# Optimization experiments

Hardware: AMD Instinct MI355X
Metric: run time of the kernel (lower is better)

Reference implementation:

```python
import jax, jax.numpy as jnp
import numpy as np

B, N, D = 128, 512, 128   # batch, nodes (= patch_len / time_window_size), feature dim (d_model_patch)
EPS = 1e-5                # torch BatchNorm1d default eps
SLOPE = 0.01              # torch F.leaky_relu default negative_slope
DIAG_INF = 1e8            # eyes_like * 100000000.0 in Dot_Graph_Construction_weights


def mask_matrix(T, decay):
    # Faithful replication of Mask_Matrix: slices i*T:(i+1)*T on a [T,T] array
    # are empty for i >= 1, so the result is all ones; we replicate exactly.
    A = np.ones((T, T), np.float32)
    for i in range(T):
        v = 0
        for r in range(i, T):
            A[i * T:(i + 1) * T, r * T:(r + 1) * T] *= decay ** v
            v += 1
        v = 0
        for r in range(i + 1):
            A[i * T:(i + 1) * T, (i - r) * T:(i - r + 1) * T] *= decay ** v
            v += 1
    return A


def setup_inputs() -> dict:
    key = jax.random.key(0)
    ks = jax.random.split(key, 3)
    s = 1.0 / np.sqrt(D)  # torch Linear default init scale
    return {
        "x": jax.random.normal(ks[0], (B, N, D), jnp.float32),
        "W_map": jax.random.uniform(ks[1], (D, D), jnp.float32, -s, s),
        "b_map": jnp.zeros((D,), jnp.float32),
        "W_theta": jax.random.uniform(ks[2], (D, D), jnp.float32, -s, s),
        "b_theta": jnp.zeros((D,), jnp.float32),
        "gamma_in": jnp.ones((D,), jnp.float32),
        "beta_in": jnp.zeros((D,), jnp.float32),
        "gamma_out": jnp.ones((D,), jnp.float32),
        "beta_out": jnp.zeros((D,), jnp.float32),
        "pre_relation": jnp.asarray(mask_matrix(N, 0.9)),
    }


def leaky_relu(x):
    return jnp.where(x >= 0, x, SLOPE * x)


def batchnorm(x, gamma, beta):
    # x: [B, N, C]; BatchNorm1d over channel C (training-mode batch stats,
    # matching torch transpose -> BN -> transpose pattern).
    mean = x.mean((0, 1))
    var = x.var((0, 1))
    return (x - mean) * jax.lax.rsqrt(var + EPS) * gamma + beta


def reference(x, W_map, b_map, W_theta, b_theta, gamma_in, beta_in,
              gamma_out, beta_out, pre_relation):
    # --- Dot_Graph_Construction_weights ---
    nf = x @ W_map + b_map                         # [B,N,D]
    adj = jnp.einsum('bnd,bmd->bnm', nf, nf)       # [B,N,N]
    eye = jnp.eye(N, dtype=x.dtype)
    adj = leaky_relu(adj - eye * DIAG_INF)
    adj = jax.nn.softmax(adj, axis=-1) + eye
    # --- decay mask (all-ones, computed faithfully) ---
    adj = adj * pre_relation
    # --- input BN ---
    xb = batchnorm(x, gamma_in, beta_in)
    # --- MPNN_mk_v2, k=1 ---
    h = jnp.einsum('bnm,bmd->bnd', adj, xb) @ W_theta + b_theta
    h = batchnorm(h, gamma_out, beta_out)
    return leaky_relu(h)                           # [B,N,D]
```

## Files before the change

### kernel.cpp

```cpp
#include <hip/hip_runtime.h>
#include <hip/hip_bf16.h>

#define B_ 128
#define N_ 512
#define D_ 128
#define M_ (B_ * N_)
#define LDSP 136

typedef unsigned short u16;
typedef short s8v __attribute__((ext_vector_type(8)));
typedef __bf16 bf8v __attribute__((ext_vector_type(8)));
typedef float f4v __attribute__((ext_vector_type(4)));

__device__ __forceinline__ float b2f(u16 v) {
  return __uint_as_float(((unsigned)v) << 16);
}
__device__ __forceinline__ u16 f2b(float f) {
  unsigned u = __float_as_uint(f);
  return (u16)((u + 0x7fffu + ((u >> 16) & 1u)) >> 16);
}
__device__ __forceinline__ void split2(float v, u16& hi, u16& lo) {
  hi = f2b(v);
  lo = f2b(v - b2f(hi));
}
__device__ __forceinline__ u16* swzK(u16* base, int row, int col) {
  return (u16*)((char*)base + row * 256 + ((col * 2) ^ ((row & 15) << 4)));
}
__device__ __forceinline__ u16* swz64(u16* base, int row, int col) {
  return (u16*)((char*)base + row * 128 + ((col * 2) ^ ((row & 7) << 4)));
}
__device__ __forceinline__ int kperm(int c) {
  return (c & 3) + ((c >> 2) & 1) * 16 + ((c >> 3) & 3) * 4 + (c >> 5) * 32;
}
__device__ __forceinline__ void derive_ss(const float* __restrict__ stats,
                                          const float* __restrict__ gamma,
                                          const float* __restrict__ beta,
                                          float* sSS, int t) {
  if (t < 128) {
    float mean = stats[t] * (1.0f / (float)M_);
    float var  = stats[128 + t] * (1.0f / (float)M_) - mean * mean;
    float sc = gamma[t] * rsqrtf(var + 1e-5f);
    sSS[t] = sc;
    sSS[128 + t] = beta[t] - mean * sc;
  }
}

__global__ __launch_bounds__(256) void prologue(const float* __restrict__ Wa,
                                                const float* __restrict__ Wb,
                                                u16* __restrict__ WTah, u16* __restrict__ WTal,
                                                u16* __restrict__ WTbh,
                                                const float* __restrict__ X,
                                                float* __restrict__ stats) {
  const int t = threadIdx.x;
  const int id = blockIdx.x;
  if (id < 128) {
    const int idx = (id & 63) * 256 + t;
    const int k = idx >> 7, j = idx & 127;
    if (id < 64) {
      u16 hh, ll;
      split2(Wa[idx], hh, ll);
      WTah[j * 128 + k] = hh;
      WTal[j * 128 + k] = ll;
    } else {
      WTbh[j * 128 + k] = f2b(Wb[idx]);
    }
    return;
  }
  const int g = t & 31;
  const int h = t >> 5;
  const size_t r0 = (size_t)(id - 128) * 256;
  float s[4] = {0.f, 0.f, 0.f, 0.f}, q[4] = {0.f, 0.f, 0.f, 0.f};
  for (int r = h; r < 256; r += 8) {
    float4 v = *(const float4*)&X[(r0 + r) * D_ + g * 4];
    s[0] += v.x; q[0] += v.x * v.x;
    s[1] += v.y; q[1] += v.y * v.y;
    s[2] += v.z; q[2] += v.z * v.z;
    s[3] += v.w; q[3] += v.w * v.w;
  }
  __shared__ float red[256][8];
#pragma unroll
  for (int j = 0; j < 4; ++j) { red[t][j] = s[j]; red[t][4 + j] = q[j]; }
  __syncthreads();
  if (t < 32) {
    float S[4] = {0.f, 0.f, 0.f, 0.f}, Q[4] = {0.f, 0.f, 0.f, 0.f};
    for (int hh = 0; hh < 8; ++hh) {
      const float* p = red[hh * 32 + t];
#pragma unroll
      for (int j = 0; j < 4; ++j) { S[j] += p[j]; Q[j] += p[4 + j]; }
    }
#pragma unroll
    for (int j = 0; j < 4; ++j) {
      atomicAdd(&stats[t * 4 + j], S[j]);
      atomicAdd(&stats[128 + t * 4 + j], Q[j]);
    }
  }
}

__global__ __launch_bounds__(256) void xbT_kernel(const float* __restrict__ X,
                                                  const float* __restrict__ stats,
                                                  const float* __restrict__ gamma,
                                                  const float* __restrict__ beta,
                                                  u16* __restrict__ XBT) {
  __shared__ __align__(16) u16 sT[128][LDSP];
  __shared__ float sSS[256];
  const int t = threadIdx.x;
  const int b = blockIdx.x >> 2;
  const int n0 = (blockIdx.x & 3) * 128;
  const size_t xbase = (size_t)b * N_ * D_;
  const size_t tbase = (size_t)b * D_ * N_;
  derive_ss(stats, gamma, beta, sSS, t);
  __syncthreads();
  {
    const int r = t >> 1, c0 = (t & 1) * 64;
#pragma unroll
    for (int i = 0; i < 16; ++i) {
      const int c = c0 + i * 4;
      float4 v = *(const float4*)&X[xbase + (size_t)(n0 + r) * D_ + c];
      sT[c + 0][r] = f2b(v.x * sSS[c + 0] + sSS[128 + c + 0]);
      sT[c + 1][r] = f2b(v.y * sSS[c + 1] + sSS[128 + c + 1]);
      sT[c + 2][r] = f2b(v.z * sSS[c + 2] + sSS[128 + c + 2]);
      sT[c + 3][r] = f2b(v.w * sSS[c + 3] + sSS[128 + c + 3]);
    }
  }
  __syncthreads();
  {
    const int d = t >> 1, nc = (t & 1) * 64;
#pragma unroll
    for (int i = 0; i < 8; ++i) {
      u16 o[8];
#pragma unroll
      for (int e = 0; e < 8; ++e) {
        const int L = nc + i * 8 + e;
        o[e] = sT[d][kperm(L & 63) + (L & 64)];
      }
      *(s8v*)&XBT[tbase + (size_t)d * N_ + n0 + nc + i * 8] = *(const s8v*)o;
    }
  }
}

__global__ __launch_bounds__(256, 2) void gemm1(const float* __restrict__ A,
                                                const u16* __restrict__ WTh,
                                                const u16* __restrict__ WTl,
                                                const float* __restrict__ bias,
                                                u16* __restrict__ Ch, u16* __restrict__ Cl) {
  __shared__ __align__(16) u16 sWh[128][LDSP];
  __shared__ __align__(16) u16 sWl[128][LDSP];
  const int t = threadIdx.x;
  const int wv = t >> 6, ln = t & 63, l16 = ln & 15, kg = ln >> 4;
  const size_t row0 = (size_t)blockIdx.x * 128;

#pragma unroll
  for (int i = 0; i < 8; ++i) {
    int o = t * 8 + i * 2048;
    int rr = o >> 7, cc = o & 127;
    *(s8v*)&sWh[rr][cc] = *(const s8v*)&WTh[o];
    *(s8v*)&sWl[rr][cc] = *(const s8v*)&WTl[o];
  }

  bf8v ah[2][4], al[2][4];
#pragma unroll
  for (int rf = 0; rf < 2; ++rf) {
    const size_t row = row0 + wv * 32 + rf * 16 + l16;
#pragma unroll
    for (int kt = 0; kt < 4; ++kt) {
      const float* p = &A[row * D_ + kt * 32 + kg * 8];
      float4 v0 = *(const float4*)p;
      float4 v1 = *(const float4*)(p + 4);
      u16 hh[8], ll[8];
      split2(v0.x, hh[0], ll[0]); split2(v0.y, hh[1], ll[1]);
      split2(v0.z, hh[2], ll[2]); split2(v0.w, hh[3], ll[3]);
      split2(v1.x, hh[4], ll[4]); split2(v1.y, hh[5], ll[5]);
      split2(v1.z, hh[6], ll[6]); split2(v1.w, hh[7], ll[7]);
      ah[rf][kt] = *(const bf8v*)hh;
      al[rf][kt] = *(const bf8v*)ll;
    }
  }
  __syncthreads();

  f4v acc[2][8];
#pragma unroll
  for (int rf = 0; rf < 2; ++rf)
#pragma unroll
    for (int jf = 0; jf < 8; ++jf) acc[rf][jf] = f4v{0.f, 0.f, 0.f, 0.f};

#pragma unroll
  for (int kt = 0; kt < 4; ++kt) {
    const int k0 = kt * 32 + kg * 8;
#pragma unroll
    for (int jf = 0; jf < 8; ++jf) {
      bf8v bh = *(const bf8v*)&sWh[jf * 16 + l16][k0];
      bf8v bl = *(const bf8v*)&sWl[jf * 16 + l16][k0];
      acc[0][jf] = __builtin_amdgcn_mfma_f32_16x16x32_bf16(ah[0][kt], bh, acc[0][jf], 0, 0, 0);
      acc[0][jf] = __builtin_amdgcn_mfma_f32_16x16x32_bf16(al[0][kt], bh, acc[0][jf], 0, 0, 0);
      acc[0][jf] = __builtin_amdgcn_mfma_f32_16x16x32_bf16(ah[0][kt], bl, acc[0][jf], 0, 0, 0);
      acc[1][jf] = __builtin_amdgcn_mfma_f32_16x16x32_bf16(ah[1][kt], bh, acc[1][jf], 0, 0, 0);
      acc[1][jf] = __builtin_amdgcn_mfma_f32_16x16x32_bf16(al[1][kt], bh, acc[1][jf], 0, 0, 0);
      acc[1][jf] = __builtin_amdgcn_mfma_f32_16x16x32_bf16(ah[1][kt], bl, acc[1][jf], 0, 0, 0);
    }
  }

#pragma unroll
  for (int rf = 0; rf < 2; ++rf) {
#pragma unroll
    for (int reg = 0; reg < 4; ++reg) {
      const int row = wv * 32 + rf * 16 + kg * 4 + reg;
#pragma unroll
      for (int jf = 0; jf < 8; ++jf) {
        const int col = jf * 16 + l16;
        float v = acc[rf][jf][reg] + bias[col];
        u16 hh, ll;
        split2(v, hh, ll);
        Ch[(row0 + row) * D_ + col] = hh;
        Cl[(row0 + row) * D_ + col] = ll;
      }
    }
  }
}

__global__ __launch_bounds__(256, 2) void gemm2(const u16* __restrict__ A,
                                                const u16* __restrict__ WTh,
                                                const float* __restrict__ bias,
                                                u16* __restrict__ C,
                                                float* __restrict__ stats) {
  __shared__ __align__(16) u16 sWh[128][LDSP];
  __shared__ float sSum[128], sSq[128];
  const int t = threadIdx.x;
  const int wv = t >> 6, ln = t & 63, l16 = ln & 15, kg = ln >> 4;
  const size_t row0 = (size_t)blockIdx.x * 128;

  if (t < 128) { sSum[t] = 0.f; sSq[t] = 0.f; }
#pragma unroll
  for (int i = 0; i < 8; ++i) {
    int o = t * 8 + i * 2048;
    *(s8v*)&sWh[o >> 7][o & 127] = *(const s8v*)&WTh[o];
  }

  bf8v a[2][4];
#pragma unroll
  for (int rf = 0; rf < 2; ++rf) {
    const size_t row = row0 + wv * 32 + rf * 16 + l16;
#pragma unroll
    for (int kt = 0; kt < 4; ++kt)
      a[rf][kt] = *(const bf8v*)&A[row * D_ + kt * 32 + kg * 8];
  }
  __syncthreads();

  f4v acc[2][8];
#pragma unroll
  for (int rf = 0; rf < 2; ++rf)
#pragma unroll
    for (int jf = 0; jf < 8; ++jf) acc[rf][jf] = f4v{0.f, 0.f, 0.f, 0.f};

#pragma unroll
  for (int kt = 0; kt < 4; ++kt) {
    const int k0 = kt * 32 + kg * 8;
#pragma unroll
    for (int jf = 0; jf < 8; ++jf) {
      bf8v bh = *(const bf8v*)&sWh[jf * 16 + l16][k0];
      acc[0][jf] = __builtin_amdgcn_mfma_f32_16x16x32_bf16(a[0][kt], bh, acc[0][jf], 0, 0, 0);
      acc[1][jf] = __builtin_amdgcn_mfma_f32_16x16x32_bf16(a[1][kt], bh, acc[1][jf], 0, 0, 0);
    }
  }

  float cs[8], cq[8];
#pragma unroll
  for (int jf = 0; jf < 8; ++jf) { cs[jf] = 0.f; cq[jf] = 0.f; }
#pragma unroll
  for (int rf = 0; rf < 2; ++rf) {
#pragma unroll
    for (int reg = 0; reg < 4; ++reg) {
      const int row = wv * 32 + rf * 16 + kg * 4 + reg;
#pragma unroll
      for (int jf = 0; jf < 8; ++jf) {
        const int col = jf * 16 + l16;
        u16 hb = f2b(acc[rf][jf][reg] + bias[col]);
        C[(row0 + row) * D_ + col] = hb;
        float vr = b2f(hb);
        cs[jf] += vr;
        cq[jf] += vr * vr;
      }
    }
  }
#pragma unroll
  for (int jf = 0; jf < 8; ++jf) {
    cs[jf] += __shfl_xor(cs[jf], 16); cq[jf] += __shfl_xor(cq[jf], 16);
    cs[jf] += __shfl_xor(cs[jf], 32); cq[jf] += __shfl_xor(cq[jf], 32);
  }
  if (kg == 0) {
#pragma unroll
    for (int jf = 0; jf < 8; ++jf) {
      atomicAdd(&sSum[jf * 16 + l16], cs[jf]);
      atomicAdd(&sSq[jf * 16 + l16], cq[jf]);
    }
  }
  __syncthreads();
  if (t < 128) {
    atomicAdd(&stats[t], sSum[t]);
    atomicAdd(&stats[128 + t], sSq[t]);
  }
}

__global__ __launch_bounds__(512, 4) void attn_kernel(const u16* __restrict__ NFH,
                                                      const u16* __restrict__ NFL,
                                                      const u16* __restrict__ XBT,
                                                      const float* __restrict__ X,
                                                      const float* __restrict__ stats,
                                                      const float* __restrict__ gamma,
                                                      const float* __restrict__ beta,
                                                      u16* __restrict__ ATT) {
  __shared__ __align__(16) u16 pool[17408];
  __shared__ float sSS[256];
  u16* sKh = pool;
  u16* sVT = pool + 8192;
  const int t = threadIdx.x;
  const int wv = t >> 6, ln = t & 63, l16 = ln & 15, kg = ln >> 4;
  const int id = blockIdx.x;
  const int b = (id & 7) + (id >> 5) * 8;
  const int r0 = ((id >> 3) & 3) * 128;
  const size_t base  = (size_t)b * N_ * D_;
  const size_t baseT = (size_t)b * D_ * N_;

  derive_ss(stats, gamma, beta, sSS, t);

  bf8v qh[4], ql[4];
  {
    const size_t qoff = base + (size_t)(r0 + wv * 16 + l16) * D_ + kg * 8;
#pragma unroll
    for (int kt = 0; kt < 4; ++kt) {
      qh[kt] = *(const bf8v*)&NFH[qoff + kt * 32];
      ql[kt] = *(const bf8v*)&NFL[qoff + kt * 32];
    }
  }

  const int kr = t >> 3, kc = (t & 7) * 16;
  const int vd = t >> 2, vc = (t & 3) * 16;
  const u16* gKh = &NFH[base + (size_t)kr * D_ + kc];
  const u16* gV  = &XBT[baseT + (size_t)vd * N_ + vc];
  s8v rh0 = *(const s8v*)gKh, rh1 = *(const s8v*)(gKh + 8);
  s8v rv0 = *(const s8v*)gV,  rv1 = *(const s8v*)(gV + 8);

  float m = -3e38f, l = 0.f;
  f4v accO[8];
#pragma unroll
  for (int df = 0; df < 8; ++df) accO[df] = f4v{0.f, 0.f, 0.f, 0.f};

  for (int j0 = 0; j0 < N_; j0 += 64) {
    *(s8v*)swzK(sKh, kr, kc)      = rh0;
    *(s8v*)swzK(sKh, kr, kc + 8)  = rh1;
    *(s8v*)swz64(sVT, vd, vc)     = rv0;
    *(s8v*)swz64(sVT, vd, vc + 8) = rv1;
    __syncthreads();
    if (j0 + 64 < N_) {
      const int jn = j0 + 64;
      rh0 = *(const s8v*)(gKh + (size_t)jn * D_);
      rh1 = *(const s8v*)(gKh + (size_t)jn * D_ + 8);
      rv0 = *(const s8v*)(gV + jn);
      rv1 = *(const s8v*)(gV + jn + 8);
    }

    f4v accS[4];
#pragma unroll
    for (int jf = 0; jf < 4; ++jf) accS[jf] = f4v{0.f, 0.f, 0.f, 0.f};
    __builtin_amdgcn_s_setprio(1);
#pragma unroll
    for (int kt = 0; kt < 4; ++kt) {
      const int k0 = kt * 32 + kg * 8;
#pragma unroll
      for (int jf = 0; jf < 4; ++jf) {
        bf8v kh_ = *(const bf8v*)swzK(sKh, jf * 16 + l16, k0);
        accS[jf] = __builtin_amdgcn_mfma_f32_16x16x32_bf16(kh_, qh[kt], accS[jf], 0, 0, 0);
        accS[jf] = __builtin_amdgcn_mfma_f32_16x16x32_bf16(kh_, ql[kt], accS[jf], 0, 0, 0);
      }
    }
    __builtin_amdgcn_s_setprio(0);

    const int qg = r0 + wv * 16 + l16;
    float mx = -3e38f;
#pragma unroll
    for (int jf = 0; jf < 4; ++jf) {
#pragma unroll
      for (int reg = 0; reg < 4; ++reg) {
        const int kk = j0 + jf * 16 + kg * 4 + reg;
        float sv = accS[jf][reg];
        if (kk == qg) sv -= 1e8f;
        sv = (sv >= 0.f) ? sv : 0.01f * sv;
        accS[jf][reg] = sv;
        mx = fmaxf(mx, sv);
      }
    }
    mx = fmaxf(mx, __shfl_xor(mx, 16));
    mx = fmaxf(mx, __shfl_xor(mx, 32));
    const bool resc = !__all(mx - m <= 8.0f);
    const float mnew = resc ? fmaxf(m, mx) : m;
    float rs = 0.f;
#pragma unroll
    for (int jf = 0; jf < 4; ++jf) {
#pragma unroll
      for (int reg = 0; reg < 4; ++reg) {
        const float p = __expf(accS[jf][reg] - mnew);
        accS[jf][reg] = p;
        rs += p;
      }
    }
    rs += __shfl_xor(rs, 16);
    rs += __shfl_xor(rs, 32);
    if (resc) {
      const float scl = __expf(m - mnew);
      l = l * scl + rs;
      m = mnew;
#pragma unroll
      for (int df = 0; df < 8; ++df) accO[df] = accO[df] * scl;
    } else {
      l += rs;
    }

    u16 pk0[8], pk1[8];
#pragma unroll
    for (int e = 0; e < 8; ++e) {
      pk0[e] = f2b(accS[(e >> 2)][e & 3]);
      pk1[e] = f2b(accS[2 + (e >> 2)][e & 3]);
    }
    bf8v pb0 = *(const bf8v*)pk0;
    bf8v pb1 = *(const bf8v*)pk1;

    __builtin_amdgcn_s_setprio(1);
#pragma unroll
    for (int kt2 = 0; kt2 < 2; ++kt2) {
      const int k0 = kt2 * 32 + kg * 8;
      const bf8v pb = kt2 ? pb1 : pb0;
#pragma unroll
      for (int df = 0; df < 8; ++df) {
        bf8v av = *(const bf8v*)swz64(sVT, df * 16 + l16, k0);
        accO[df] = __builtin_amdgcn_mfma_f32_16x16x32_bf16(av, pb, accO[df], 0, 0, 0);
      }
    }
    __builtin_amdgcn_s_setprio(0);
    __syncthreads();
  }

  const float inv = 1.0f / l;
  u16* sOut = pool;
#pragma unroll
  for (int df = 0; df < 8; ++df) {
#pragma unroll
    for (int reg = 0; reg < 4; ++reg) {
      const int d = df * 16 + kg * 4 + reg;
      sOut[d * 136 + wv * 16 + l16] = f2b(accO[df][reg] * inv);
    }
  }
  __syncthreads();
  {
    const int q = t >> 2, c0 = (t & 3) * 32;
    const size_t orow = base + (size_t)(r0 + q) * D_;
#pragma unroll
    for (int i = 0; i < 4; ++i) {
      u16 o[8];
#pragma unroll
      for (int e = 0; e < 8; ++e) {
        const int d = c0 + i * 8 + e;
        const float ov = b2f(sOut[d * 136 + q]);
        const float xb = X[orow + d] * sSS[d] + sSS[128 + d];
        o[e] = f2b(ov + xb);
      }
      *(s8v*)&ATT[orow + c0 + i * 8] = *(const s8v*)o;
    }
  }
}

__global__ __launch_bounds__(256) void affine_out(const u16* __restrict__ H,
                                                  const float* __restrict__ stats,
                                                  const float* __restrict__ gamma,
                                                  const float* __restrict__ beta,
                                                  float* __restrict__ Y) {
  __shared__ float sSS[256];
  const int t = threadIdx.x;
  derive_ss(stats, gamma, beta, sSS, t);
  __syncthreads();
  const size_t idx = (size_t)blockIdx.x * 256 + t;
  const int c0 = (int)(idx & 15) * 8;
  s8v v = *(const s8v*)&H[idx * 8];
  float o[8];
#pragma unroll
  for (int e = 0; e < 8; ++e) {
    float x = b2f((u16)v[e]);
    float y = x * sSS[c0 + e] + sSS[128 + c0 + e];
    o[e] = (y >= 0.f) ? y : 0.01f * y;
  }
  *(float4*)&Y[idx * 8]     = make_float4(o[0], o[1], o[2], o[3]);
  *(float4*)&Y[idx * 8 + 4] = make_float4(o[4], o[5], o[6], o[7]);
}

extern "C" void kernel_launch(void* const* d_in, const int* in_sizes, int n_in,
                              void* d_out, int out_size, void* d_ws, size_t ws_size,
                              hipStream_t stream) {
  const float* x         = (const float*)d_in[0];
  const float* W_map     = (const float*)d_in[1];
  const float* b_map     = (const float*)d_in[2];
  const float* W_theta   = (const float*)d_in[3];
  const float* b_theta   = (const float*)d_in[4];
  const float* gamma_in  = (const float*)d_in[5];
  const float* beta_in   = (const float*)d_in[6];
  const float* gamma_out = (const float*)d_in[7];
  const float* beta_out  = (const float*)d_in[8];
  float* out = (float*)d_out;

  char* ws = (char*)d_ws;
  float* stats_x = (float*)ws;
  float* stats_h = (float*)(ws + 1024);
  u16* WT1h = (u16*)(ws + 2048);
  u16* WT1l = WT1h + 128 * 128;
  u16* WT2h = WT1l + 128 * 128;
  const size_t BUF = (size_t)M_ * D_;
  u16* nfh = WT2h + 128 * 128;
  u16* nfl = nfh + BUF;

  u16* xbT  = (u16*)d_out;
  u16* attO = (u16*)d_out + BUF;

  hipMemsetAsync(ws, 0, 2048, stream);

  prologue<<<384, 256, 0, stream>>>(W_map, W_theta, WT1h, WT1l, WT2h, x, stats_x);
  gemm1<<<512, 256, 0, stream>>>(x, WT1h, WT1l, b_map, nfh, nfl);
  xbT_kernel<<<512, 256, 0, stream>>>(x, stats_x, gamma_in, beta_in, xbT);
  attn_kernel<<<512, 512, 0, stream>>>(nfh, nfl, xbT, x, stats_x, gamma_in, beta_in, attO);
  gemm2<<<512, 256, 0, stream>>>(attO, WT2h, b_theta, nfh, stats_h);
  affine_out<<<4096, 256, 0, stream>>>(nfh, stats_h, gamma_out, beta_out, out);
}
```

Baseline: 158.1 us.

## Fuse xbT into gemm1, stage GEMM outputs via LDS, simplify attention inner loop

Removes the separate xbT kernel: gemm1 now computes the normalized transposed bf16 input from its already-loaded hi/lo A fragments and writes XBT, avoiding a second read of x. gemm1 and gemm2 stage outputs in LDS and write coalesced 16-byte rows instead of scattered 2-byte stores. In attention, the diagonal-mask comparison runs only for the tile containing the query row, and the P conversion uses packed v_cvt_pk_bf16_f32. Reconstructing x from hi+lo bf16 may differ slightly from the fp32 original, and the extra syncs and LDS reuse add some overhead to gemm1.

```diff
diff --git a/kernel.cpp b/kernel.cpp
--- a/kernel.cpp
+++ b/kernel.cpp
@@ -11,6 +11,7 @@
 typedef short s8v __attribute__((ext_vector_type(8)));
 typedef __bf16 bf8v __attribute__((ext_vector_type(8)));
 typedef float f4v __attribute__((ext_vector_type(4)));
+typedef unsigned u4v __attribute__((ext_vector_type(4)));
 
 __device__ __forceinline__ float b2f(u16 v) {
   return __uint_as_float(((unsigned)v) << 16);
@@ -22,6 +23,11 @@
 __device__ __forceinline__ void split2(float v, u16& hi, u16& lo) {
   hi = f2b(v);
   lo = f2b(v - b2f(hi));
+}
+__device__ __forceinline__ unsigned cvtpk(float lo, float hi) {
+  unsigned r;
+  asm("v_cvt_pk_bf16_f32 %0, %1, %2" : "=v"(r) : "v"(lo), "v"(hi));
+  return r;
 }
 __device__ __forceinline__ u16* swzK(u16* base, int row, int col) {
   return (u16*)((char*)base + row * 256 + ((col * 2) ^ ((row & 15) << 4)));
@@ -96,58 +102,26 @@
   }
 }
 
-__global__ __launch_bounds__(256) void xbT_kernel(const float* __restrict__ X,
-                                                  const float* __restrict__ stats,
-                                                  const float* __restrict__ gamma,
-                                                  const float* __restrict__ beta,
-                                                  u16* __restrict__ XBT) {
-  __shared__ __align__(16) u16 sT[128][LDSP];
-  __shared__ float sSS[256];
-  const int t = threadIdx.x;
-  const int b = blockIdx.x >> 2;
-  const int n0 = (blockIdx.x & 3) * 128;
-  const size_t xbase = (size_t)b * N_ * D_;
-  const size_t tbase = (size_t)b * D_ * N_;
-  derive_ss(stats, gamma, beta, sSS, t);
-  __syncthreads();
-  {
-    const int r = t >> 1, c0 = (t & 1) * 64;
-#pragma unroll
-    for (int i = 0; i < 16; ++i) {
-      const int c = c0 + i * 4;
-      float4 v = *(const float4*)&X[xbase + (size_t)(n0 + r) * D_ + c];
-      sT[c + 0][r] = f2b(v.x * sSS[c + 0] + sSS[128 + c + 0]);
-      sT[c + 1][r] = f2b(v.y * sSS[c + 1] + sSS[128 + c + 1]);
-      sT[c + 2][r] = f2b(v.z * sSS[c + 2] + sSS[128 + c + 2]);
-      sT[c + 3][r] = f2b(v.w * sSS[c + 3] + sSS[128 + c + 3]);
-    }
-  }
-  __syncthreads();
-  {
-    const int d = t >> 1, nc = (t & 1) * 64;
-#pragma unroll
-    for (int i = 0; i < 8; ++i) {
-      u16 o[8];
-#pragma unroll
-      for (int e = 0; e < 8; ++e) {
-        const int L = nc + i * 8 + e;
-        o[e] = sT[d][kperm(L & 63) + (L & 64)];
-      }
-      *(s8v*)&XBT[tbase + (size_t)d * N_ + n0 + nc + i * 8] = *(const s8v*)o;
-    }
-  }
-}
-
 __global__ __launch_bounds__(256, 2) void gemm1(const float* __restrict__ A,
                                                 const u16* __restrict__ WTh,
                                                 const u16* __restrict__ WTl,
                                                 const float* __restrict__ bias,
-                                                u16* __restrict__ Ch, u16* __restrict__ Cl) {
-  __shared__ __align__(16) u16 sWh[128][LDSP];
-  __shared__ __align__(16) u16 sWl[128][LDSP];
+                                                u16* __restrict__ Ch, u16* __restrict__ Cl,
+                                                const float* __restrict__ stats,
+                                                const float* __restrict__ gamma,
+                                                const float* __restrict__ beta,
+                                                u16* __restrict__ XBT) {
+  __shared__ __align__(16) u16 pool[2 * 128 * LDSP];
+  __shared__ float sSS[256];
+  u16 (*sWh)[LDSP] = (u16(*)[LDSP])pool;
+  u16 (*sWl)[LDSP] = (u16(*)[LDSP])(pool + 128 * LDSP);
   const int t = threadIdx.x;
   const int wv = t >> 6, ln = t & 63, l16 = ln & 15, kg = ln >> 4;
   const size_t row0 = (size_t)blockIdx.x * 128;
+  const int b = blockIdx.x >> 2;
+  const int n0 = (blockIdx.x & 3) * 128;
+
+  derive_ss(stats, gamma, beta, sSS, t);
 
 #pragma unroll
   for (int i = 0; i < 8; ++i) {
@@ -199,6 +173,9 @@
     }
   }
 
+  __syncthreads();
+  u16 (*cH)[LDSP] = sWh;
+  u16 (*cL)[LDSP] = sWl;
 #pragma unroll
   for (int rf = 0; rf < 2; ++rf) {
 #pragma unroll
@@ -210,9 +187,49 @@
         float v = acc[rf][jf][reg] + bias[col];
         u16 hh, ll;
         split2(v, hh, ll);
-        Ch[(row0 + row) * D_ + col] = hh;
-        Cl[(row0 + row) * D_ + col] = ll;
-      }
+        cH[row][col] = hh;
+        cL[row][col] = ll;
+      }
+    }
+  }
+  __syncthreads();
+  {
+    const int r = t >> 1, c0 = (t & 1) * 64;
+#pragma unroll
+    for (int i = 0; i < 8; ++i) {
+      *(s8v*)&Ch[(row0 + r) * D_ + c0 + i * 8] = *(const s8v*)&cH[r][c0 + i * 8];
+      *(s8v*)&Cl[(row0 + r) * D_ + c0 + i * 8] = *(const s8v*)&cL[r][c0 + i * 8];
+    }
+  }
+
+  __syncthreads();
+  u16 (*sT)[LDSP] = sWh;
+#pragma unroll
+  for (int rf = 0; rf < 2; ++rf) {
+    const int nl = wv * 32 + rf * 16 + l16;
+#pragma unroll
+    for (int kt = 0; kt < 4; ++kt) {
+#pragma unroll
+      for (int e = 0; e < 8; ++e) {
+        const int d = kt * 32 + kg * 8 + e;
+        const float xv = (float)ah[rf][kt][e] + (float)al[rf][kt][e];
+        sT[d][nl] = f2b(xv * sSS[d] + sSS[128 + d]);
+      }
+    }
+  }
+  __syncthreads();
+  {
+    const size_t tbase = (size_t)b * D_ * N_;
+    const int d = t >> 1, nc = (t & 1) * 64;
+#pragma unroll
+    for (int i = 0; i < 8; ++i) {
+      u16 o[8];
+#pragma unroll
+      for (int e = 0; e < 8; ++e) {
+        const int L = nc + i * 8 + e;
+        o[e] = sT[d][kperm(L & 63) + (L & 64)];
+      }
+      *(s8v*)&XBT[tbase + (size_t)d * N_ + n0 + nc + i * 8] = *(const s8v*)o;
     }
   }
 }
@@ -262,6 +279,8 @@
     }
   }
 
+  __syncthreads();
+  u16 (*cT)[LDSP] = sWh;
   float cs[8], cq[8];
 #pragma unroll
   for (int jf = 0; jf < 8; ++jf) { cs[jf] = 0.f; cq[jf] = 0.f; }
@@ -274,7 +293,7 @@
       for (int jf = 0; jf < 8; ++jf) {
         const int col = jf * 16 + l16;
         u16 hb = f2b(acc[rf][jf][reg] + bias[col]);
-        C[(row0 + row) * D_ + col] = hb;
+        cT[row][col] = hb;
         float vr = b2f(hb);
         cs[jf] += vr;
         cq[jf] += vr * vr;
@@ -294,6 +313,12 @@
     }
   }
   __syncthreads();
+  {
+    const int r = t >> 1, c0 = (t & 1) * 64;
+#pragma unroll
+    for (int i = 0; i < 8; ++i)
+      *(s8v*)&C[(row0 + r) * D_ + c0 + i * 8] = *(const s8v*)&cT[r][c0 + i * 8];
+  }
   if (t < 128) {
     atomicAdd(&stats[t], sSum[t]);
     atomicAdd(&stats[128 + t], sSq[t]);
@@ -344,6 +369,9 @@
 #pragma unroll
   for (int df = 0; df < 8; ++df) accO[df] = f4v{0.f, 0.f, 0.f, 0.f};
 
+  const int qg = r0 + wv * 16 + l16;
+  const int qtile = qg & ~63;
+
   for (int j0 = 0; j0 < N_; j0 += 64) {
     *(s8v*)swzK(sKh, kr, kc)      = rh0;
     *(s8v*)swzK(sKh, kr, kc + 8)  = rh1;
@@ -374,18 +402,30 @@
     }
     __builtin_amdgcn_s_setprio(0);
 
-    const int qg = r0 + wv * 16 + l16;
     float mx = -3e38f;
-#pragma unroll
-    for (int jf = 0; jf < 4; ++jf) {
-#pragma unroll
-      for (int reg = 0; reg < 4; ++reg) {
-        const int kk = j0 + jf * 16 + kg * 4 + reg;
-        float sv = accS[jf][reg];
-        if (kk == qg) sv -= 1e8f;
-        sv = (sv >= 0.f) ? sv : 0.01f * sv;
-        accS[jf][reg] = sv;
-        mx = fmaxf(mx, sv);
+    if (j0 == qtile) {
+#pragma unroll
+      for (int jf = 0; jf < 4; ++jf) {
+#pragma unroll
+        for (int reg = 0; reg < 4; ++reg) {
+          const int kk = j0 + jf * 16 + kg * 4 + reg;
+          float sv = accS[jf][reg];
+          if (kk == qg) sv -= 1e8f;
+          sv = (sv >= 0.f) ? sv : 0.01f * sv;
+          accS[jf][reg] = sv;
+          mx = fmaxf(mx, sv);
+        }
+      }
+    } else {
+#pragma unroll
+      for (int jf = 0; jf < 4; ++jf) {
+#pragma unroll
+        for (int reg = 0; reg < 4; ++reg) {
+          float sv = accS[jf][reg];
+          sv = (sv >= 0.f) ? sv : 0.01f * sv;
+          accS[jf][reg] = sv;
+          mx = fmaxf(mx, sv);
+        }
       }
     }
     mx = fmaxf(mx, __shfl_xor(mx, 16));
@@ -414,14 +454,18 @@
       l += rs;
     }
 
-    u16 pk0[8], pk1[8];
-#pragma unroll
-    for (int e = 0; e < 8; ++e) {
-      pk0[e] = f2b(accS[(e >> 2)][e & 3]);
-      pk1[e] = f2b(accS[2 + (e >> 2)][e & 3]);
-    }
-    bf8v pb0 = *(const bf8v*)pk0;
-    bf8v pb1 = *(const bf8v*)pk1;
+    u4v w0, w1;
+    w0[0] = cvtpk(accS[0][0], accS[0][1]);
+    w0[1] = cvtpk(accS[0][2], accS[0][3]);
+    w0[2] = cvtpk(accS[1][0], accS[1][1]);
+    w0[3] = cvtpk(accS[1][2], accS[1][3]);
+    w1[0] = cvtpk(accS[2][0], accS[2][1]);
+    w1[1] = cvtpk(accS[2][2], accS[2][3]);
+    w1[2] = cvtpk(accS[3][0], accS[3][1]);
+    w1[3] = cvtpk(accS[3][2], accS[3][3]);
+    bf8v pb0, pb1;
+    __builtin_memcpy(&pb0, &w0, 16);
+    __builtin_memcpy(&pb1, &w1, 16);
 
     __builtin_amdgcn_s_setprio(1);
 #pragma unroll
@@ -520,8 +564,8 @@
   hipMemsetAsync(ws, 0, 2048, stream);
 
   prologue<<<384, 256, 0, stream>>>(W_map, W_theta, WT1h, WT1l, WT2h, x, stats_x);
-  gemm1<<<512, 256, 0, stream>>>(x, WT1h, WT1l, b_map, nfh, nfl);
-  xbT_kernel<<<512, 256, 0, stream>>>(x, stats_x, gamma_in, beta_in, xbT);
+  gemm1<<<512, 256, 0, stream>>>(x, WT1h, WT1l, b_map, nfh, nfl,
+                                 stats_x, gamma_in, beta_in, xbT);
   attn_kernel<<<512, 512, 0, stream>>>(nfh, nfl, xbT, x, stats_x, gamma_in, beta_in, attO);
   gemm2<<<512, 256, 0, stream>>>(attO, WT2h, b_theta, nfh, stats_h);
   affine_out<<<4096, 256, 0, stream>>>(nfh, stats_h, gamma_out, beta_out, out);
```

Result: no change. 155.9 us (-1.4%).
